# Kernel tuning notes

Hardware: AMD Instinct MI355X
Metric: run time of the kernel (lower is better)

The kernel has to match this reference:

```python
import jax, jax.numpy as jnp
import numpy as np

TEMP = 0.1
EPS = 1e-12  # F.normalize eps


def setup_inputs() -> dict:
    key = jax.random.key(0)
    k1, k2 = jax.random.split(key)
    B, C, N = 8, 128, 4096
    features = jax.random.normal(k1, (B, C, N), dtype=jnp.float32)
    labels_all = jax.random.randint(k2, (B, N), 0, 16, dtype=jnp.int32)
    return {"features": features, "labels_all": labels_all}


def _per_cloud_loss(features_map, labels):
    # features_map: [C, N], labels: [N]
    v = features_map.T  # [N, C]
    v = v / jnp.maximum(jnp.linalg.norm(v, axis=1, keepdims=True), EPS)
    dp = jnp.exp(jnp.matmul(v, v.T) / TEMP)  # [N, N]
    n = dp.shape[0]
    # remove diagonal (dot_products - diag(diagonal))
    dp = dp * (1.0 - jnp.eye(n, dtype=dp.dtype))
    mask = labels[:, None] == labels[None, :]  # [N, N]
    positives = jnp.sum(jnp.where(mask, dp, 0.0), axis=1)
    negatives = jnp.sum(jnp.where(mask, 0.0, dp), axis=1)
    deviation = -jnp.log(positives / (positives + negatives))
    return jnp.mean(deviation)


def reference(features, labels_all):
    # features: [B, C, N], labels_all: [B, N]
    losses = jax.vmap(_per_cloud_loss)(features, labels_all)  # [B]
    return jnp.mean(losses)
```

## Files before the change

kernel.cpp:

```cpp
#include <hip/hip_runtime.h>
#include <hip/hip_bf16.h>
#include <math.h>

#define BATCH 8
#define NPTS 4096
#define CH 128

#define SQRT_TEMP_LOG2E 3.79828256f

typedef __attribute__((ext_vector_type(4))) float f32x4;
typedef __attribute__((ext_vector_type(4))) int   i32x4;
typedef __attribute__((ext_vector_type(8))) short bf16x8;

typedef __attribute__((address_space(3))) unsigned int lds_uint;
typedef __attribute__((address_space(1))) const unsigned int gbl_uint;

__device__ __forceinline__ void load_lds16(const void* g, const void* l) {
    __builtin_amdgcn_global_load_lds((gbl_uint*)g, (lds_uint*)l, 16, 0, 0);
}

__device__ __forceinline__ float fast_exp2(float x) {
    return __builtin_amdgcn_exp2f(x);
}

__global__ __launch_bounds__(256) void normalize_kernel(
    const float* __restrict__ f, __hip_bfloat16* __restrict__ vn,
    float* __restrict__ pos, float* __restrict__ neg)
{
    int idx = blockIdx.x * 256 + threadIdx.x;
    int point = idx >> 2, q = idx & 3;
    int b = point >> 12, n = point & (NPTS - 1);
    const float* base = f + (size_t)b * CH * NPTS + (size_t)(q * 32) * NPTS + n;

    float x[32];
    float ss = 0.0f;
    #pragma unroll
    for (int c = 0; c < 32; c++) {
        x[c] = base[(size_t)c * NPTS];
        ss += x[c] * x[c];
    }
    ss += __shfl_xor(ss, 1);
    ss += __shfl_xor(ss, 2);
    float scale = SQRT_TEMP_LOG2E / fmaxf(sqrtf(ss), 1e-12f);

    __hip_bfloat16* out = vn + (size_t)point * CH + q * 32;
    #pragma unroll
    for (int c0 = 0; c0 < 32; c0 += 8) {
        union { __hip_bfloat16 h[8]; uint4 u; } pk;
        #pragma unroll
        for (int j = 0; j < 8; j++)
            pk.h[j] = __float2bfloat16(x[c0 + j] * scale);
        *((uint4*)(out + c0)) = pk.u;
    }
    if (q == 0) pos[point] = 0.0f;
    else if (q == 1) neg[point] = 0.0f;
}

__global__ __launch_bounds__(256, 4) void tile_kernel(
    const __hip_bfloat16* __restrict__ vn, const int* __restrict__ labels,
    float* __restrict__ pos, float* __restrict__ neg)
{
    __shared__ short lB[128 * CH];
    __shared__ int labC[128];

    const int b  = blockIdx.z;
    const int rt = blockIdx.y, ct = blockIdx.x;
    const bool diag = (rt == ct);

    const int tid = threadIdx.x;
    const int w = tid >> 6, lane = tid & 63;
    const int lane15 = lane & 15, quad = lane >> 4;

    const int row0 = rt * 128, col0 = ct * 128;
    const __hip_bfloat16* vb = vn + (size_t)b * NPTS * CH;

    if (tid < 128) labC[tid] = labels[b * NPTS + col0 + tid];

    {
        const __hip_bfloat16* Bb = vb + (size_t)col0 * CH;
        #pragma unroll
        for (int i = 0; i < 8; i++) {
            int ldsrow = (w * 8 + i) * 4;
            int r = ldsrow + quad;
            int g = lane15 ^ (r & 15);
            load_lds16(Bb + (size_t)r * CH + g * 8, &lB[ldsrow * CH]);
        }
    }

    bf16x8 afrag[2][4];
    int lr[2];
    #pragma unroll
    for (int mi = 0; mi < 2; mi++) {
        const int row_l = w * 32 + mi * 16 + lane15;
        const __hip_bfloat16* Arow = vb + (size_t)(row0 + row_l) * CH;
        #pragma unroll
        for (int ks = 0; ks < 4; ks++)
            afrag[mi][ks] = *(const bf16x8*)(Arow + (ks * 4 + quad) * 8);
        lr[mi] = labels[b * NPTS + row0 + row_l];
    }

    __syncthreads();

    f32x4 acc[2][8] = {};
    #pragma unroll
    for (int ks = 0; ks < 4; ks++) {
        const int koff = ((ks * 4 + quad) ^ lane15) << 3;
        #pragma unroll
        for (int ni = 0; ni < 8; ni++) {
            bf16x8 bf = *(const bf16x8*)&lB[(ni * 16 + lane15) * CH + koff];
            acc[0][ni] = __builtin_amdgcn_mfma_f32_16x16x32_bf16(
                bf, afrag[0][ks], acc[0][ni], 0, 0, 0);
            acc[1][ni] = __builtin_amdgcn_mfma_f32_16x16x32_bf16(
                bf, afrag[1][ks], acc[1][ni], 0, 0, 0);
        }
    }

    #pragma unroll
    for (int mi = 0; mi < 2; mi++) {
        const int row_l = w * 32 + mi * 16 + lane15;
        float p = 0.0f, tt = 0.0f;
        if (diag) {
            #pragma unroll
            for (int ni = 0; ni < 8; ni++) {
                const bool dblk = (ni * 16 == w * 32 + mi * 16);
                const i32x4 lc = *(const i32x4*)&labC[ni * 16 + quad * 4];
                #pragma unroll
                for (int r = 0; r < 4; r++) {
                    float e = fast_exp2(acc[mi][ni][r]);
                    if (dblk && lane15 == quad * 4 + r) e = 0.0f;
                    tt += e;
                    p  += (lc[r] == lr[mi]) ? e : 0.0f;
                }
            }
        } else {
            #pragma unroll
            for (int ni = 0; ni < 8; ni++) {
                const i32x4 lc = *(const i32x4*)&labC[ni * 16 + quad * 4];
                #pragma unroll
                for (int r = 0; r < 4; r++) {
                    float e = fast_exp2(acc[mi][ni][r]);
                    tt += e;
                    p  += (lc[r] == lr[mi]) ? e : 0.0f;
                }
            }
        }
        p  += __shfl_xor(p, 16);   p  += __shfl_xor(p, 32);
        tt += __shfl_xor(tt, 16);  tt += __shfl_xor(tt, 32);
        if (lane < 16) {
            atomicAdd(&pos[b * NPTS + row0 + row_l], p);
            atomicAdd(&neg[b * NPTS + row0 + row_l], tt - p);
        }
    }
}

__global__ __launch_bounds__(1024) void finalize_kernel(
    const float* __restrict__ pos, const float* __restrict__ neg,
    float* __restrict__ out)
{
    float acc = 0.0f;
    for (int i = threadIdx.x; i < BATCH * NPTS; i += 1024) {
        float p = pos[i];
        float t = p + neg[i];
        acc += __logf(t / p);
    }
    #pragma unroll
    for (int off = 32; off; off >>= 1) acc += __shfl_down(acc, off);
    __shared__ float red[16];
    if ((threadIdx.x & 63) == 0) red[threadIdx.x >> 6] = acc;
    __syncthreads();
    if (threadIdx.x < 16) {
        float v = red[threadIdx.x];
        #pragma unroll
        for (int off = 8; off; off >>= 1) v += __shfl_down(v, off);
        if (threadIdx.x == 0) out[0] = v * (1.0f / (BATCH * NPTS));
    }
}

extern "C" void kernel_launch(void* const* d_in, const int* in_sizes, int n_in,
                              void* d_out, int out_size, void* d_ws, size_t ws_size,
                              hipStream_t stream)
{
    const float* features = (const float*)d_in[0];
    const int*   labels   = (const int*)d_in[1];
    float*       out      = (float*)d_out;

    __hip_bfloat16* vn = (__hip_bfloat16*)d_ws;
    float* pos = (float*)((char*)d_ws + (size_t)BATCH * NPTS * CH * sizeof(__hip_bfloat16));
    float* neg = pos + BATCH * NPTS;

    hipLaunchKernelGGL(normalize_kernel, dim3(BATCH * NPTS * 4 / 256), dim3(256), 0, stream,
                       features, vn, pos, neg);
    hipLaunchKernelGGL(tile_kernel, dim3(32, 32, BATCH), dim3(256), 0, stream,
                       vn, labels, pos, neg);
    hipLaunchKernelGGL(finalize_kernel, dim3(1), dim3(1024), 0, stream, pos, neg, out);
}
```

Before: 127.5 us.

## Loop batches inside persistent tile blocks and prefetch next batch during epilogue

The tile kernel now launches 1024 blocks, one per row/column tile pair, and each block loops over all 8 batches instead of using a 3D grid with one block per batch. While the exp/label epilogue of the current batch runs, the B tile for the next batch is loaded into LDS asynchronously, and the A fragments and labels are loaded into registers. Label buffers are double-buffered. This aims to hide global load latency behind compute and cut block launch overhead. In exchange the grid has 8x fewer blocks, so occupancy and tail balance depend on 1024 blocks filling the GPU, and register pressure rises from holding both the accumulators and the next batch's fragments.

```diff
diff --git a/kernel.cpp b/kernel.cpp
--- a/kernel.cpp
+++ b/kernel.cpp
@@ -61,23 +61,18 @@
     float* __restrict__ pos, float* __restrict__ neg)
 {
     __shared__ short lB[128 * CH];
-    __shared__ int labC[128];
-
-    const int b  = blockIdx.z;
-    const int rt = blockIdx.y, ct = blockIdx.x;
+    __shared__ int labC[2][128];
+
+    const int rt = blockIdx.x >> 5, ct = blockIdx.x & 31;
     const bool diag = (rt == ct);
+    const int row0 = rt * 128, col0 = ct * 128;
 
     const int tid = threadIdx.x;
     const int w = tid >> 6, lane = tid & 63;
     const int lane15 = lane & 15, quad = lane >> 4;
 
-    const int row0 = rt * 128, col0 = ct * 128;
-    const __hip_bfloat16* vb = vn + (size_t)b * NPTS * CH;
-
-    if (tid < 128) labC[tid] = labels[b * NPTS + col0 + tid];
-
     {
-        const __hip_bfloat16* Bb = vb + (size_t)col0 * CH;
+        const __hip_bfloat16* Bb = vn + (size_t)col0 * CH;
         #pragma unroll
         for (int i = 0; i < 8; i++) {
             int ldsrow = (w * 8 + i) * 4;
@@ -86,69 +81,99 @@
             load_lds16(Bb + (size_t)r * CH + g * 8, &lB[ldsrow * CH]);
         }
     }
+    if (tid < 128) labC[0][tid] = labels[col0 + tid];
 
     bf16x8 afrag[2][4];
     int lr[2];
     #pragma unroll
     for (int mi = 0; mi < 2; mi++) {
         const int row_l = w * 32 + mi * 16 + lane15;
-        const __hip_bfloat16* Arow = vb + (size_t)(row0 + row_l) * CH;
+        const __hip_bfloat16* Arow = vn + (size_t)(row0 + row_l) * CH;
         #pragma unroll
         for (int ks = 0; ks < 4; ks++)
             afrag[mi][ks] = *(const bf16x8*)(Arow + (ks * 4 + quad) * 8);
-        lr[mi] = labels[b * NPTS + row0 + row_l];
-    }
-
-    __syncthreads();
-
-    f32x4 acc[2][8] = {};
-    #pragma unroll
-    for (int ks = 0; ks < 4; ks++) {
-        const int koff = ((ks * 4 + quad) ^ lane15) << 3;
-        #pragma unroll
-        for (int ni = 0; ni < 8; ni++) {
-            bf16x8 bf = *(const bf16x8*)&lB[(ni * 16 + lane15) * CH + koff];
-            acc[0][ni] = __builtin_amdgcn_mfma_f32_16x16x32_bf16(
-                bf, afrag[0][ks], acc[0][ni], 0, 0, 0);
-            acc[1][ni] = __builtin_amdgcn_mfma_f32_16x16x32_bf16(
-                bf, afrag[1][ks], acc[1][ni], 0, 0, 0);
-        }
-    }
-
-    #pragma unroll
-    for (int mi = 0; mi < 2; mi++) {
-        const int row_l = w * 32 + mi * 16 + lane15;
-        float p = 0.0f, tt = 0.0f;
-        if (diag) {
+        lr[mi] = labels[row0 + row_l];
+    }
+
+    for (int b = 0; b < BATCH; b++) {
+        __syncthreads();
+
+        f32x4 acc[2][8] = {};
+        #pragma unroll
+        for (int ks = 0; ks < 4; ks++) {
+            const int koff = ((ks * 4 + quad) ^ lane15) << 3;
             #pragma unroll
             for (int ni = 0; ni < 8; ni++) {
-                const bool dblk = (ni * 16 == w * 32 + mi * 16);
-                const i32x4 lc = *(const i32x4*)&labC[ni * 16 + quad * 4];
+                bf16x8 bf = *(const bf16x8*)&lB[(ni * 16 + lane15) * CH + koff];
+                acc[0][ni] = __builtin_amdgcn_mfma_f32_16x16x32_bf16(
+                    bf, afrag[0][ks], acc[0][ni], 0, 0, 0);
+                acc[1][ni] = __builtin_amdgcn_mfma_f32_16x16x32_bf16(
+                    bf, afrag[1][ks], acc[1][ni], 0, 0, 0);
+            }
+        }
+
+        __syncthreads();
+
+        const int buf = b & 1;
+        int lr_cur[2] = { lr[0], lr[1] };
+
+        if (b + 1 < BATCH) {
+            const __hip_bfloat16* vb_n = vn + (size_t)(b + 1) * NPTS * CH;
+            const __hip_bfloat16* Bb = vb_n + (size_t)col0 * CH;
+            #pragma unroll
+            for (int i = 0; i < 8; i++) {
+                int ldsrow = (w * 8 + i) * 4;
+                int r = ldsrow + quad;
+                int g = lane15 ^ (r & 15);
+                load_lds16(Bb + (size_t)r * CH + g * 8, &lB[ldsrow * CH]);
+            }
+            if (tid < 128) labC[buf ^ 1][tid] = labels[(b + 1) * NPTS + col0 + tid];
+            #pragma unroll
+            for (int mi = 0; mi < 2; mi++) {
+                const int row_l = w * 32 + mi * 16 + lane15;
+                const __hip_bfloat16* Arow = vb_n + (size_t)(row0 + row_l) * CH;
                 #pragma unroll
-                for (int r = 0; r < 4; r++) {
-                    float e = fast_exp2(acc[mi][ni][r]);
-                    if (dblk && lane15 == quad * 4 + r) e = 0.0f;
-                    tt += e;
-                    p  += (lc[r] == lr[mi]) ? e : 0.0f;
+                for (int ks = 0; ks < 4; ks++)
+                    afrag[mi][ks] = *(const bf16x8*)(Arow + (ks * 4 + quad) * 8);
+                lr[mi] = labels[(b + 1) * NPTS + row0 + row_l];
+            }
+        }
+
+        #pragma unroll
+        for (int mi = 0; mi < 2; mi++) {
+            const int row_l = w * 32 + mi * 16 + lane15;
+            float p = 0.0f, tt = 0.0f;
+            if (diag) {
+                #pragma unroll
+                for (int ni = 0; ni < 8; ni++) {
+                    const bool dblk = (ni * 16 == w * 32 + mi * 16);
+                    const i32x4 lc = *(const i32x4*)&labC[buf][ni * 16 + quad * 4];
+                    #pragma unroll
+                    for (int r = 0; r < 4; r++) {
+                        float e = fast_exp2(acc[mi][ni][r]);
+                        if (dblk && lane15 == quad * 4 + r) e = 0.0f;
+                        tt += e;
+                        p  += (lc[r] == lr_cur[mi]) ? e : 0.0f;
+                    }
                 }
-            }
-        } else {
-            #pragma unroll
-            for (int ni = 0; ni < 8; ni++) {
-                const i32x4 lc = *(const i32x4*)&labC[ni * 16 + quad * 4];
+            } else {
                 #pragma unroll
-                for (int r = 0; r < 4; r++) {
-                    float e = fast_exp2(acc[mi][ni][r]);
-                    tt += e;
-                    p  += (lc[r] == lr[mi]) ? e : 0.0f;
+                for (int ni = 0; ni < 8; ni++) {
+                    const i32x4 lc = *(const i32x4*)&labC[buf][ni * 16 + quad * 4];
+                    #pragma unroll
+                    for (int r = 0; r < 4; r++) {
+                        float e = fast_exp2(acc[mi][ni][r]);
+                        tt += e;
+                        p  += (lc[r] == lr_cur[mi]) ? e : 0.0f;
+                    }
                 }
             }
-        }
-        p  += __shfl_xor(p, 16);   p  += __shfl_xor(p, 32);
-        tt += __shfl_xor(tt, 16);  tt += __shfl_xor(tt, 32);
-        if (lane < 16) {
-            atomicAdd(&pos[b * NPTS + row0 + row_l], p);
-            atomicAdd(&neg[b * NPTS + row0 + row_l], tt - p);
+            p  += __shfl_xor(p, 16);   p  += __shfl_xor(p, 32);
+            tt += __shfl_xor(tt, 16);  tt += __shfl_xor(tt, 32);
+            if (lane < 16) {
+                atomicAdd(&pos[b * NPTS + row0 + row_l], p);
+                atomicAdd(&neg[b * NPTS + row0 + row_l], tt - p);
+            }
         }
     }
 }
@@ -190,7 +215,7 @@
 
     hipLaunchKernelGGL(normalize_kernel, dim3(BATCH * NPTS * 4 / 256), dim3(256), 0, stream,
                        features, vn, pos, neg);
-    hipLaunchKernelGGL(tile_kernel, dim3(32, 32, BATCH), dim3(256), 0, stream,
+    hipLaunchKernelGGL(tile_kernel, dim3(1024), dim3(256), 0, stream,
                        vn, labels, pos, neg);
     hipLaunchKernelGGL(finalize_kernel, dim3(1), dim3(1024), 0, stream, pos, neg, out);
 }
```

New measurement: 200.0 us. 56.8% more time.
